# Performance work log

Hardware: AMD Instinct MI355X
Metric: run time of the kernel (lower is better)

Reference implementation:

```python
import jax, jax.numpy as jnp
import numpy as np

EPS = 1e-12
W_MAX = 0.8
ALPHA_MAX = 1.5
T = 10
ETA = 0.2
ALPHA_SCALE = 1.0
N = 50000
IN_DIM = 512
HID = 256
C = 8
EH = 64
E2 = 400000  # undirected pairs; E = 2*E2 directed edges


def setup_inputs() -> dict:
    key = jax.random.key(0)
    ks = jax.random.split(key, 12)
    x = jax.random.normal(ks[0], (N, IN_DIM), jnp.float32)
    src0 = jax.random.randint(ks[1], (E2,), 0, N)
    dst0 = jax.random.randint(ks[2], (E2,), 0, N)
    edge_index = jnp.concatenate([jnp.stack([src0, dst0]), jnp.stack([dst0, src0])], axis=1)
    rev = jnp.concatenate([jnp.arange(E2) + E2, jnp.arange(E2)])
    def lin(k, i, o):
        return jax.random.normal(k, (i, o), jnp.float32) * (2.0 / i) ** 0.5
    enc_w1 = lin(ks[3], IN_DIM, HID); enc_b1 = jnp.zeros((HID,), jnp.float32)
    enc_w2 = lin(ks[4], HID, C); enc_b2 = jnp.zeros((C,), jnp.float32)
    edge_w1 = lin(ks[5], 2 * HID + 2, EH); edge_b1 = jnp.zeros((EH,), jnp.float32)
    edge_w2 = lin(ks[6], EH, 1); edge_b2 = jnp.zeros((1,), jnp.float32)
    bound = (6.0 / (C + C)) ** 0.5  # xavier_uniform
    R_raw = jax.random.uniform(ks[7], (C, C), jnp.float32, -bound, bound) + 0.5 * jnp.eye(C, dtype=jnp.float32)
    R_scale_log = jnp.float32(0.0)
    msg_logit = jnp.float32(-3.0)
    return dict(x=x, edge_index=edge_index, rev=rev,
                enc_w1=enc_w1, enc_b1=enc_b1, enc_w2=enc_w2, enc_b2=enc_b2,
                edge_w1=edge_w1, edge_b1=edge_b1, edge_w2=edge_w2, edge_b2=edge_b2,
                R_raw=R_raw, R_scale_log=R_scale_log, msg_logit=msg_logit)


def reference(x, edge_index, rev, enc_w1, enc_b1, enc_w2, enc_b2,
              edge_w1, edge_b1, edge_w2, edge_b2, R_raw, R_scale_log, msg_logit):
    num_nodes = x.shape[0]
    src, dst = edge_index[0], edge_index[1]
    # unary encoder (mlp type, eval mode -> no dropout)
    h = jax.nn.relu(x @ enc_w1 + enc_b1)
    logits = h @ enc_w2 + enc_b2
    log_phi = jax.nn.log_softmax(logits, axis=-1)  # [N, C]
    # structural edge features from out-degree of src
    deg = jax.ops.segment_sum(jnp.ones_like(src, jnp.float32), src, num_segments=num_nodes)
    logdeg = jnp.log(deg + 1.0)
    a, b = logdeg[src], logdeg[dst]
    struct = jnp.stack([a + b, jnp.abs(a - b)], axis=-1)  # [E, 2]
    # learned symmetric edge weights -> per-edge kernel K
    hs, hd = h[src], h[dst]
    edge_in = jnp.concatenate([hs * hd, jnp.abs(hs - hd), struct], axis=-1)  # [E, 2H+2]
    eh = jax.nn.relu(edge_in @ edge_w1 + edge_b1)
    w_raw = (eh @ edge_w2 + edge_b2)[:, 0]
    w = W_MAX * jax.nn.sigmoid(w_raw)
    w = 0.5 * (w + w[rev])
    R = 0.5 * (R_raw + R_raw.T)
    R = (jax.nn.softplus(R_scale_log) + 1e-06) * jnp.tanh(R)
    K = jnp.exp(w[:, None, None] * R[None])  # [E, C, C]
    degc = jnp.maximum(deg, 1.0)
    edge_norm = (degc[src] * degc[dst]) ** -0.5  # [E]
    alpha = ALPHA_MAX * jax.nn.sigmoid(msg_logit) * ALPHA_SCALE
    lp_src = log_phi[src]
    m = jax.nn.softmax(lp_src, axis=-1)  # init_unary=True

    def step(m, _):
        f = jnp.einsum('ec,ecd->ed', m, K)
        log_f = jnp.log(jnp.maximum(f, EPS)) * edge_norm[:, None]
        sum_in = jax.ops.segment_sum(log_f, dst, num_segments=num_nodes)
        excl = sum_in[src] - log_f[rev]
        m_new = jax.nn.softmax(lp_src + alpha * excl, axis=-1)
        m = (1.0 - ETA) * m + ETA * m_new
        m = jnp.maximum(m, EPS)
        m = m / m.sum(axis=-1, keepdims=True)
        return m, None

    m, _ = jax.lax.scan(step, m, None, length=T)
    # beliefs
    f = jnp.einsum('ec,ecd->ed', m, K)
    log_f = jnp.log(jnp.maximum(f, EPS)) * edge_norm[:, None]
    sum_in = jax.ops.segment_sum(log_f, dst, num_segments=num_nodes)
    beliefs = jax.nn.softmax(log_phi + alpha * sum_in, axis=-1)
    return beliefs
```

## Files before the change

kernel.cpp:

```cpp
#include <hip/hip_runtime.h>
#include <cstddef>
#include <cstdint>

typedef _Float16 h4 __attribute__((ext_vector_type(4)));
typedef _Float16 h8 __attribute__((ext_vector_type(8)));
typedef float    f4 __attribute__((ext_vector_type(4)));
typedef int      i4 __attribute__((ext_vector_type(4)));

#define NN      50000
#define IND     512
#define HIDN    256
#define E2P     400000
#define EDD     800000
#define NBLK    196
#define SCN     50176
#define EBLK    1563

#define OFF_HF16    ((size_t)0)
#define OFF_LOGF    ((size_t)0)
#define OFF_Z       ((size_t)25600000)
#define OFF_DEG     ((size_t)28800000)
#define OFF_LOGDEG  ((size_t)29004800)
#define OFF_DEGC    ((size_t)29204800)
#define OFF_BASE    ((size_t)29404800)
#define OFF_CNT     ((size_t)29609600)
#define OFF_BLK     ((size_t)29814400)
#define OFF_WT      ((size_t)29818496)
#define OFF_BT      ((size_t)30080640)
#define OFF_RS      ((size_t)30150272)
#define OFF_WSYM    ((size_t)30150784)
#define OFF_POS     ((size_t)31750784)
#define OFF_ORDER   ((size_t)34950784)
#define OFF_BASE2   ((size_t)36550784)
#define OFF_OFS2    ((size_t)36755584)
#define OFF_PRC     ((size_t)36960384)
#define OFF_WN      ((size_t)43360384)
#define OFF_M       ((size_t)46560384)
#define OFF_EIS     ((size_t)59360384)
#define WS_NEED     ((size_t)62560384)

__device__ __forceinline__ int key2(int s, int d) {
    return ((s >> 10) << 10) | (d >> 6);
}

__device__ __forceinline__ int xcd_swz(int bid, int nwg) {
    int q = nwg >> 3, r = nwg & 7;
    int x = bid & 7, idx = bid >> 3;
    return (x < r ? x * (q + 1) : r * (q + 1) + (x - r) * q) + idx;
}

__global__ void k_deg(const int* __restrict__ ei, int* __restrict__ deg,
                      int* __restrict__ cnt2) {
    int e = blockIdx.x * 256 + threadIdx.x;
    int v = ei[e];
    atomicAdd(&deg[v], 1);
    if (e < E2P) {
        int d = ei[EDD + e];
        atomicAdd(&cnt2[key2(v, d)], 1);
    }
}

__global__ void k_node(const int* __restrict__ deg, float* __restrict__ logdeg,
                       float* __restrict__ degc) {
    int n = blockIdx.x * 256 + threadIdx.x;
    if (n < NN) {
        float d = (float)deg[n];
        logdeg[n] = logf(d + 1.0f);
        degc[n]   = fmaxf(d, 1.0f);
    }
}

__global__ void k_scan1(const int* __restrict__ deg, int* __restrict__ incl,
                        int* __restrict__ blk) {
    __shared__ int sm[256];
    int i = blockIdx.x * 256 + threadIdx.x;
    int v = deg[i];
    sm[threadIdx.x] = v;
    __syncthreads();
    for (int off = 1; off < 256; off <<= 1) {
        int t = (threadIdx.x >= off) ? sm[threadIdx.x - off] : 0;
        __syncthreads();
        sm[threadIdx.x] += t;
        __syncthreads();
    }
    incl[i] = sm[threadIdx.x];
    if (threadIdx.x == 255) blk[blockIdx.x] = sm[255];
}

__global__ void k_scan2(int* __restrict__ blk) {
    __shared__ int sm[256];
    int v = (threadIdx.x < NBLK) ? blk[threadIdx.x] : 0;
    sm[threadIdx.x] = v;
    __syncthreads();
    for (int off = 1; off < 256; off <<= 1) {
        int t = (threadIdx.x >= off) ? sm[threadIdx.x - off] : 0;
        __syncthreads();
        sm[threadIdx.x] += t;
        __syncthreads();
    }
    if (threadIdx.x < NBLK) blk[threadIdx.x] = sm[threadIdx.x];
}

__global__ void k_scan3(const int* __restrict__ incl, const int* __restrict__ deg,
                        const int* __restrict__ blk, int* __restrict__ base) {
    int i = blockIdx.x * 256 + threadIdx.x;
    int off = (blockIdx.x > 0) ? blk[blockIdx.x - 1] : 0;
    base[i] = off + incl[i] - deg[i];
}

__global__ void k_pos(const int* __restrict__ ei, const int* __restrict__ base,
                      int* __restrict__ cnt, int* __restrict__ pos) {
    int e = blockIdx.x * 256 + threadIdx.x;
    int dstn = ei[EDD + e];
    pos[e] = base[dstn] + atomicAdd(&cnt[dstn], 1);
}

__global__ void k_order(const int* __restrict__ ei, const int* __restrict__ base2,
                        int* __restrict__ ofs2, int* __restrict__ order) {
    int p = blockIdx.x * 256 + threadIdx.x;
    if (p < E2P) {
        int k = key2(ei[p], ei[EDD + p]);
        order[base2[k] + atomicAdd(&ofs2[k], 1)] = p;
    }
}

__global__ void k_gath(const int* __restrict__ ei, const int* __restrict__ order,
                       int2* __restrict__ eiS) {
    int i = blockIdx.x * 256 + threadIdx.x;
    if (i < E2P) {
        int p = order[i];
        eiS[i] = make_int2(ei[p], ei[EDD + p]);
    }
}

__global__ void k_prep(const float* __restrict__ enc_w1, const float* __restrict__ edge_w1,
                       const float* __restrict__ R_raw, const float* __restrict__ Rsl,
                       const float* __restrict__ mlog,
                       _Float16* __restrict__ Wt, _Float16* __restrict__ Bt,
                       float* __restrict__ Rs) {
    int gid = blockIdx.x * 256 + threadIdx.x;
    if (gid < 256 * 512) {
        int n = gid >> 9, k = gid & 511;
        Wt[n * 512 + k] = (_Float16)enc_w1[k * 256 + n];
        return;
    }
    int g2 = gid - 256 * 512;
    if (g2 < 64 * 544) {
        int n = g2 / 544, k = g2 - n * 544;
        float v = 0.0f;
        if (k < 512) {
            int tm = k >> 5, r = k & 31;
            int qq = r >> 3, jj = (r >> 1) & 3, typ = k & 1;
            int c = (tm >> 1) * 32 + qq * 8 + (tm & 1) * 4 + jj;
            v = edge_w1[(typ ? 256 + c : c) * 64 + n];
        } else if (k < 514) {
            v = edge_w1[k * 64 + n];
        }
        Bt[n * 544 + k] = (_Float16)v;
        return;
    }
    int g3 = g2 - 64 * 544;
    if (g3 < 64) {
        int c = g3 >> 3, d = g3 & 7;
        float rv = 0.5f * (R_raw[c * 8 + d] + R_raw[d * 8 + c]);
        float s  = log1pf(expf(Rsl[0])) + 1e-6f;
        Rs[g3] = s * tanhf(rv);
        return;
    }
    if (g3 == 64) {
        Rs[64] = 1.5f / (1.0f + expf(-mlog[0]));
    }
}

__global__ __launch_bounds__(256) void k_enc(const float* __restrict__ x,
                                             const _Float16* __restrict__ Wt,
                                             const float* __restrict__ b1,
                                             _Float16* __restrict__ hf) {
    __shared__ _Float16 XL[32 * 32];
    __shared__ _Float16 WL[256 * 32];
    const int tid = threadIdx.x;
    const int wid = tid >> 6;
    const int lane = tid & 63;
    const int l15 = lane & 15;
    const int q = lane >> 4;
    const int m0 = blockIdx.x * 32;
    const int mt = wid & 1;
    const int nh = wid >> 1;

    f4 acc[8];
#pragma unroll
    for (int i = 0; i < 8; i++) acc[i] = (f4){0.f, 0.f, 0.f, 0.f};

    const int xr = tid >> 2;
    const int xs = tid & 3;
    const bool xact = (tid < 128);
    const int gr = m0 + xr;

    h8 xreg = (h8){0, 0, 0, 0, 0, 0, 0, 0};
    if (xact && gr < NN) {
        const f4* xp = (const f4*)(x + (size_t)gr * IND + xs * 8);
        f4 a0 = xp[0], a1 = xp[1];
#pragma unroll
        for (int u = 0; u < 4; u++) { xreg[u] = (_Float16)a0[u]; xreg[4 + u] = (_Float16)a1[u]; }
    }
    h8 wreg[4];
#pragma unroll
    for (int rep = 0; rep < 4; rep++) {
        int id = rep * 256 + tid;
        int n = id >> 2, c = id & 3;
        wreg[rep] = *(const h8*)(Wt + (size_t)n * IND + c * 8);
    }

    for (int kt = 0; kt < 16; kt++) {
        __syncthreads();
        if (xact) *(h8*)&XL[xr * 32 + ((xs + (xr >> 1)) & 3) * 8] = xreg;
#pragma unroll
        for (int rep = 0; rep < 4; rep++) {
            int id = rep * 256 + tid;
            int n = id >> 2, c = id & 3;
            *(h8*)&WL[n * 32 + ((c + (n >> 1)) & 3) * 8] = wreg[rep];
        }
        __syncthreads();
        if (kt < 15) {
            const int kc = (kt + 1) * 32;
            if (xact && gr < NN) {
                const f4* xp = (const f4*)(x + (size_t)gr * IND + kc + xs * 8);
                f4 a0 = xp[0], a1 = xp[1];
#pragma unroll
                for (int u = 0; u < 4; u++) { xreg[u] = (_Float16)a0[u]; xreg[4 + u] = (_Float16)a1[u]; }
            }
#pragma unroll
            for (int rep = 0; rep < 4; rep++) {
                int id = rep * 256 + tid;
                int n = id >> 2, c = id & 3;
                wreg[rep] = *(const h8*)(Wt + (size_t)n * IND + kc + c * 8);
            }
        }
        const int ar = mt * 16 + l15;
        h8 a = *(const h8*)&XL[ar * 32 + ((q + (ar >> 1)) & 3) * 8];
#pragma unroll
        for (int nt8 = 0; nt8 < 8; nt8++) {
            int r2 = (nh * 8 + nt8) * 16 + l15;
            h8 b = *(const h8*)&WL[r2 * 32 + ((q + (r2 >> 1)) & 3) * 8];
            acc[nt8] = __builtin_amdgcn_mfma_f32_16x16x32_f16(a, b, acc[nt8], 0, 0, 0);
        }
    }
#pragma unroll
    for (int nt8 = 0; nt8 < 8; nt8++) {
        int col = (nh * 8 + nt8) * 16 + l15;
        float bv = b1[col];
#pragma unroll
        for (int reg = 0; reg < 4; reg++) {
            int row = m0 + mt * 16 + q * 4 + reg;
            if (row < NN) {
                float v = acc[nt8][reg] + bv;
                hf[(size_t)row * HIDN + col] = (_Float16)fmaxf(v, 0.f);
            }
        }
    }
}

__global__ void k_logits(const _Float16* __restrict__ hf, const float* __restrict__ w2,
                         const float* __restrict__ b2, float* __restrict__ Z) {
    __shared__ float w2L[2048];
    for (int i = threadIdx.x; i < 2048; i += 256) w2L[i] = w2[i];
    __syncthreads();
    int n = blockIdx.x * 256 + threadIdx.x;
    if (n >= NN) return;
    float sum[8];
#pragma unroll
    for (int c = 0; c < 8; c++) sum[c] = b2[c];
    for (int kb = 0; kb < 32; kb++) {
        h8 hv = *(const h8*)(hf + (size_t)n * HIDN + kb * 8);
#pragma unroll
        for (int u = 0; u < 8; u++) {
            float hx = (float)hv[u];
            const float* wr = &w2L[(kb * 8 + u) * 8];
#pragma unroll
            for (int c = 0; c < 8; c++) sum[c] += hx * wr[c];
        }
    }
    float mx = sum[0];
#pragma unroll
    for (int c = 1; c < 8; c++) mx = fmaxf(mx, sum[c]);
    float se = 0.f;
#pragma unroll
    for (int c = 0; c < 8; c++) se += __expf(sum[c] - mx);
    float lse = __logf(se);
#pragma unroll
    for (int c = 0; c < 8; c++) Z[(size_t)n * 16 + c] = sum[c] - mx - lse;
}

__global__ __launch_bounds__(256) void k_edge(const int2* __restrict__ eiS,
        const _Float16* __restrict__ hf, const float* __restrict__ logdeg,
        const _Float16* __restrict__ BtG, const float* __restrict__ eb1,
        const float* __restrict__ ew2, const float* __restrict__ eb2,
        float* __restrict__ wsym2) {
    __shared__ _Float16 BtL[64 * 136];
    const int tid = threadIdx.x;
    const int wid = tid >> 6;
    const int lane = tid & 63;
    const int l15 = lane & 15;
    const int q = lane >> 4;
    const int eb = xcd_swz(blockIdx.x, gridDim.x) * 128;

    int sidx[2], didx[2];
    float la[2], lb[2];
#pragma unroll
    for (int mt = 0; mt < 2; mt++) {
        int e = eb + wid * 32 + mt * 16 + l15;
        int2 sd = eiS[e];
        sidx[mt] = sd.x;
        didx[mt] = sd.y;
        la[mt] = logdeg[sidx[mt]];
        lb[mt] = logdeg[didx[mt]];
    }

    f4 acc[2][4];
#pragma unroll
    for (int a = 0; a < 2; a++)
#pragma unroll
        for (int b = 0; b < 4; b++) acc[a][b] = (f4){0.f, 0.f, 0.f, 0.f};

    const _Float16* hq = hf + q * 8;
    h8 curS[2], curD[2];
#pragma unroll
    for (int mt = 0; mt < 2; mt++) {
        curS[mt] = *(const h8*)(hq + (size_t)sidx[mt] * HIDN);
        curD[mt] = *(const h8*)(hq + (size_t)didx[mt] * HIDN);
    }

    for (int ph = 0; ph < 4; ph++) {
        __syncthreads();
        {
            const int r = tid >> 2;
            const int c0 = tid & 3;
            const int kbase = ph * 128;
#pragma unroll
            for (int i2 = 0; i2 < 4; i2++) {
                int ck = c0 + i2 * 4;
                *(h8*)&BtL[r * 136 + ck * 8] =
                    *(const h8*)(BtG + (size_t)r * 544 + kbase + ck * 8);
            }
        }
        __syncthreads();
#pragma unroll
        for (int kk2 = 0; kk2 < 2; kk2++) {
            const int kk = ph * 2 + kk2;
            h8 nxtS[2], nxtD[2];
            if (kk < 7) {
                const int c1 = (kk + 1) * 32;
#pragma unroll
                for (int mt = 0; mt < 2; mt++) {
                    nxtS[mt] = *(const h8*)(hq + (size_t)sidx[mt] * HIDN + c1);
                    nxtD[mt] = *(const h8*)(hq + (size_t)didx[mt] * HIDN + c1);
                }
            }
            const int ko = kk2 * 64 + q * 8;
            {
                h8 a0[2];
#pragma unroll
                for (int mt = 0; mt < 2; mt++) {
#pragma unroll
                    for (int j = 0; j < 4; j++) {
                        float x1 = (float)curS[mt][j], x2 = (float)curD[mt][j];
                        a0[mt][2 * j]     = (_Float16)(x1 * x2);
                        a0[mt][2 * j + 1] = (_Float16)fabsf(x1 - x2);
                    }
                }
                h8 bf[4];
#pragma unroll
                for (int nt = 0; nt < 4; nt++)
                    bf[nt] = *(const h8*)&BtL[(nt * 16 + l15) * 136 + ko];
#pragma unroll
                for (int mt = 0; mt < 2; mt++)
#pragma unroll
                    for (int nt = 0; nt < 4; nt++)
                        acc[mt][nt] = __builtin_amdgcn_mfma_f32_16x16x32_f16(a0[mt], bf[nt], acc[mt][nt], 0, 0, 0);
            }
            {
                h8 a1[2];
#pragma unroll
                for (int mt = 0; mt < 2; mt++) {
#pragma unroll
                    for (int j = 0; j < 4; j++) {
                        float x1 = (float)curS[mt][4 + j], x2 = (float)curD[mt][4 + j];
                        a1[mt][2 * j]     = (_Float16)(x1 * x2);
                        a1[mt][2 * j + 1] = (_Float16)fabsf(x1 - x2);
                    }
                }
                h8 bf[4];
#pragma unroll
                for (int nt = 0; nt < 4; nt++)
                    bf[nt] = *(const h8*)&BtL[(nt * 16 + l15) * 136 + ko + 32];
#pragma unroll
                for (int mt = 0; mt < 2; mt++)
#pragma unroll
                    for (int nt = 0; nt < 4; nt++)
                        acc[mt][nt] = __builtin_amdgcn_mfma_f32_16x16x32_f16(a1[mt], bf[nt], acc[mt][nt], 0, 0, 0);
            }
            if (kk < 7) {
#pragma unroll
                for (int mt = 0; mt < 2; mt++) { curS[mt] = nxtS[mt]; curD[mt] = nxtD[mt]; }
            }
        }
    }

    __syncthreads();
    {
        const int r = tid >> 2, ck = tid & 3;
        *(h8*)&BtL[r * 136 + ck * 8] = *(const h8*)(BtG + (size_t)r * 544 + 512 + ck * 8);
    }
    __syncthreads();
    {
        h8 bf[4];
#pragma unroll
        for (int nt = 0; nt < 4; nt++)
            bf[nt] = *(const h8*)&BtL[(nt * 16 + l15) * 136 + q * 8];
#pragma unroll
        for (int mt = 0; mt < 2; mt++) {
            h8 a = (h8){0, 0, 0, 0, 0, 0, 0, 0};
            if (q == 0) {
                a[0] = (_Float16)(la[mt] + lb[mt]);
                a[1] = (_Float16)fabsf(la[mt] - lb[mt]);
            }
#pragma unroll
            for (int nt = 0; nt < 4; nt++)
                acc[mt][nt] = __builtin_amdgcn_mfma_f32_16x16x32_f16(a, bf[nt], acc[mt][nt], 0, 0, 0);
        }
    }

    float b1v[4], w2v[4];
#pragma unroll
    for (int nt = 0; nt < 4; nt++) {
        int col = nt * 16 + l15;
        b1v[nt] = eb1[col];
        w2v[nt] = ew2[col];
    }
    const float b2s = eb2[0];
    float part[2][4];
#pragma unroll
    for (int mt = 0; mt < 2; mt++)
#pragma unroll
        for (int reg = 0; reg < 4; reg++) {
            float s = 0.f;
#pragma unroll
            for (int nt = 0; nt < 4; nt++) {
                float v = acc[mt][nt][reg] + b1v[nt];
                s += fmaxf(v, 0.f) * w2v[nt];
            }
            part[mt][reg] = s;
        }
#pragma unroll
    for (int off = 1; off < 16; off <<= 1)
#pragma unroll
        for (int mt = 0; mt < 2; mt++)
#pragma unroll
            for (int reg = 0; reg < 4; reg++)
                part[mt][reg] += __shfl_xor(part[mt][reg], off, 64);
    if (l15 == 0) {
#pragma unroll
        for (int mt = 0; mt < 2; mt++)
#pragma unroll
            for (int reg = 0; reg < 4; reg++) {
                int er = eb + wid * 32 + mt * 16 + q * 4 + reg;
                if (er < E2P) {
                    float xr = part[mt][reg] + b2s;
                    wsym2[er] = 0.8f / (1.0f + __expf(-xr));
                }
            }
    }
}


__device__ __forceinline__ void kprod(const float* __restrict__ RsL, float w,
                                      const float* me, const float* mr,
                                      float* fe, float* fr) {
#pragma unroll
    for (int d = 0; d < 8; d++) { fe[d] = 0.f; fr[d] = 0.f; }
#pragma unroll
    for (int c = 0; c < 8; c++) {
        {
            float kv = __expf(w * RsL[c * 8 + c]);
            fe[c] += me[c] * kv;
            fr[c] += mr[c] * kv;
        }
#pragma unroll
        for (int d = c + 1; d < 8; d++) {
            float kv = __expf(w * RsL[c * 8 + d]);
            fe[d] += me[c] * kv; fr[d] += mr[c] * kv;
            fe[c] += me[d] * kv; fr[c] += mr[d] * kv;
        }
    }
}

__global__ __launch_bounds__(256) void k_init(const int2* __restrict__ eiS,
        const float* __restrict__ wsym2, const float* __restrict__ degc,
        const float* __restrict__ Rs, const float* __restrict__ Z,
        const int* __restrict__ pos, const int* __restrict__ order,
        i4* __restrict__ prc, float2* __restrict__ wn,
        _Float16* __restrict__ M, _Float16* __restrict__ logf) {
    __shared__ float RsL[64];
    const int tid = threadIdx.x;
    if (tid < 64) RsL[tid] = Rs[tid];
    __syncthreads();
    int i = xcd_swz(blockIdx.x, EBLK) * 256 + tid;
    if (i >= E2P) return;
    int p = order[i];
    int2 sd = eiS[i];
    int sp = sd.x, dp = sd.y;
    float w = wsym2[i];
    float nrm = rsqrtf(degc[sp] * degc[dp]);
    int pz0 = pos[p], pz1 = pos[E2P + p];
    prc[i] = (i4){sp, dp, pz0, pz1};
    wn[i] = make_float2(w, nrm);
    const f4* Zs = (const f4*)(Z + (size_t)sp * 16);
    const f4* Zd = (const f4*)(Z + (size_t)dp * 16);
    f4 ls0 = Zs[0], ls1 = Zs[1], ld0 = Zd[0], ld1 = Zd[1];
    float lps[8], lpd[8];
#pragma unroll
    for (int u = 0; u < 4; u++) { lps[u] = ls0[u]; lps[4+u] = ls1[u]; lpd[u] = ld0[u]; lpd[4+u] = ld1[u]; }
    float me[8], mr[8];
    {
        float mx = lps[0], mx2 = lpd[0];
#pragma unroll
        for (int d = 1; d < 8; d++) { mx = fmaxf(mx, lps[d]); mx2 = fmaxf(mx2, lpd[d]); }
        float s = 0.f, s2 = 0.f;
#pragma unroll
        for (int d = 0; d < 8; d++) { me[d] = __expf(lps[d] - mx); s += me[d];
                                      mr[d] = __expf(lpd[d] - mx2); s2 += mr[d]; }
        float rs = 1.f / s, rs2 = 1.f / s2;
#pragma unroll
        for (int d = 0; d < 8; d++) { me[d] *= rs; mr[d] *= rs2; }
    }
    {
        h8 mh, mh2;
#pragma unroll
        for (int d = 0; d < 8; d++) { mh[d] = (_Float16)me[d]; mh2[d] = (_Float16)mr[d]; }
        *(h8*)(M + (size_t)i * 16)     = mh;
        *(h8*)(M + (size_t)i * 16 + 8) = mh2;
    }
    float fe[8], fr[8];
    kprod(RsL, w, me, mr, fe, fr);
    h8 le, lr;
#pragma unroll
    for (int d = 0; d < 8; d++) {
        le[d] = (_Float16)(__logf(fmaxf(fe[d], 1e-12f)) * nrm);
        lr[d] = (_Float16)(__logf(fmaxf(fr[d], 1e-12f)) * nrm);
    }
    *(h8*)(logf + (size_t)pz0 * 8) = le;
    *(h8*)(logf + (size_t)pz1 * 8) = lr;
}

__global__ __launch_bounds__(256) void k_bpF(const i4* __restrict__ prc,
        const float2* __restrict__ wn, const float* __restrict__ Rs,
        const float* __restrict__ Z, _Float16* __restrict__ M,
        _Float16* __restrict__ logf) {
    __shared__ float RsL[64];
    const int tid = threadIdx.x;
    if (tid < 64) RsL[tid] = Rs[tid];
    __syncthreads();
    int i = xcd_swz(blockIdx.x, EBLK) * 256 + tid;
    if (i >= E2P) return;
    i4 c4 = prc[i];
    const int sp = c4[0], dp = c4[1], pz0 = c4[2], pz1 = c4[3];
    float2 wnv = wn[i];
    const float w = wnv.x, nrm = wnv.y;
    const float alpha = Rs[64];
    h8 mhe = *(const h8*)(M + (size_t)i * 16);
    h8 mhr = *(const h8*)(M + (size_t)i * 16 + 8);
    float me[8], mr[8];
#pragma unroll
    for (int d = 0; d < 8; d++) { me[d] = (float)mhe[d]; mr[d] = (float)mhr[d]; }
    float fe[8], fr[8];
    kprod(RsL, w, me, mr, fe, fr);
    float lfe[8], lfr[8];
#pragma unroll
    for (int d = 0; d < 8; d++) {
        lfe[d] = __logf(fmaxf(fe[d], 1e-12f)) * nrm;
        lfr[d] = __logf(fmaxf(fr[d], 1e-12f)) * nrm;
    }
    const f4* Zs = (const f4*)(Z + (size_t)sp * 16);
    const f4* Zd = (const f4*)(Z + (size_t)dp * 16);
    f4 ls0 = Zs[0], ls1 = Zs[1], ss0 = Zs[2], ss1 = Zs[3];
    f4 ld0 = Zd[0], ld1 = Zd[1], sd0 = Zd[2], sd1 = Zd[3];
    float te[8], tr[8];
#pragma unroll
    for (int u = 0; u < 4; u++) {
        te[u]     = ls0[u] + alpha * (ss0[u] - lfr[u]);
        te[4 + u] = ls1[u] + alpha * (ss1[u] - lfr[4 + u]);
        tr[u]     = ld0[u] + alpha * (sd0[u] - lfe[u]);
        tr[4 + u] = ld1[u] + alpha * (sd1[u] - lfe[4 + u]);
    }
    float m1[8], m2[8];
    {
        float mx = te[0], mx2 = tr[0];
#pragma unroll
        for (int d = 1; d < 8; d++) { mx = fmaxf(mx, te[d]); mx2 = fmaxf(mx2, tr[d]); }
        float s = 0.f, s2 = 0.f;
#pragma unroll
        for (int d = 0; d < 8; d++) { m1[d] = __expf(te[d] - mx); s += m1[d];
                                      m2[d] = __expf(tr[d] - mx2); s2 += m2[d]; }
        float rs = 1.f / s, rs2 = 1.f / s2;
        float t1 = 0.f, t2 = 0.f;
#pragma unroll
        for (int d = 0; d < 8; d++) {
            m1[d] = fmaxf(0.8f * me[d] + 0.2f * m1[d] * rs, 1e-12f);  t1 += m1[d];
            m2[d] = fmaxf(0.8f * mr[d] + 0.2f * m2[d] * rs2, 1e-12f); t2 += m2[d];
        }
        float rt1 = 1.f / t1, rt2 = 1.f / t2;
#pragma unroll
        for (int d = 0; d < 8; d++) { m1[d] *= rt1; m2[d] *= rt2; }
    }
    {
        h8 mh, mh2;
#pragma unroll
        for (int d = 0; d < 8; d++) { mh[d] = (_Float16)m1[d]; mh2[d] = (_Float16)m2[d]; }
        *(h8*)(M + (size_t)i * 16)     = mh;
        *(h8*)(M + (size_t)i * 16 + 8) = mh2;
    }
    float fe2[8], fr2[8];
    kprod(RsL, w, m1, m2, fe2, fr2);
    h8 le, lr;
#pragma unroll
    for (int d = 0; d < 8; d++) {
        le[d] = (_Float16)(__logf(fmaxf(fe2[d], 1e-12f)) * nrm);
        lr[d] = (_Float16)(__logf(fmaxf(fr2[d], 1e-12f)) * nrm);
    }
    *(h8*)(logf + (size_t)pz0 * 8) = le;
    *(h8*)(logf + (size_t)pz1 * 8) = lr;
}

__global__ void k_sum(const _Float16* __restrict__ logf, const int* __restrict__ base,
                      const int* __restrict__ deg, float* __restrict__ Z,
                      const float* __restrict__ Rs, float* __restrict__ out, int fin) {
    int g = blockIdx.x * 256 + threadIdx.x;
    int n = g >> 3;
    if (n >= NN) return;
    int j = threadIdx.x & 7;
    int b = base[n], cnt = deg[n];
    float acc[8];
#pragma unroll
    for (int d = 0; d < 8; d++) acc[d] = 0.f;
    for (int s = j; s < cnt; s += 8) {
        h8 v = *(const h8*)(logf + (size_t)(b + s) * 8);
#pragma unroll
        for (int d = 0; d < 8; d++) acc[d] += (float)v[d];
    }
    int lane = threadIdx.x & 63;
    float v4[4], v2[2], r;
    {
        bool hi = (lane & 4) != 0;
#pragma unroll
        for (int i = 0; i < 4; i++) {
            float send = hi ? acc[i] : acc[i + 4];
            float recv = __shfl_xor(send, 4, 64);
            v4[i] = (hi ? acc[i + 4] : acc[i]) + recv;
        }
    }
    {
        bool hi = (lane & 2) != 0;
#pragma unroll
        for (int i = 0; i < 2; i++) {
            float send = hi ? v4[i] : v4[i + 2];
            float recv = __shfl_xor(send, 2, 64);
            v2[i] = (hi ? v4[i + 2] : v4[i]) + recv;
        }
    }
    {
        bool hi = (lane & 1) != 0;
        float send = hi ? v2[0] : v2[1];
        float recv = __shfl_xor(send, 1, 64);
        r = (hi ? v2[1] : v2[0]) + recv;
    }
    if (!fin) {
        Z[(size_t)n * 16 + 8 + j] = r;
    } else {
        float alpha = Rs[64];
        float v = Z[(size_t)n * 16 + j] + alpha * r;
        float mx = v;
        mx = fmaxf(mx, __shfl_xor(mx, 1, 64));
        mx = fmaxf(mx, __shfl_xor(mx, 2, 64));
        mx = fmaxf(mx, __shfl_xor(mx, 4, 64));
        float ex = __expf(v - mx);
        float s = ex;
        s += __shfl_xor(s, 1, 64); s += __shfl_xor(s, 2, 64); s += __shfl_xor(s, 4, 64);
        out[(size_t)n * 8 + j] = ex / s;
    }
}

extern "C" void kernel_launch(void* const* d_in, const int* in_sizes, int n_in,
                              void* d_out, int out_size, void* d_ws, size_t ws_size,
                              hipStream_t stream) {
    if (ws_size < WS_NEED) return;
    const float* x        = (const float*)d_in[0];
    const int*   ei       = (const int*)d_in[1];
    const float* enc_w1   = (const float*)d_in[3];
    const float* enc_b1   = (const float*)d_in[4];
    const float* enc_w2   = (const float*)d_in[5];
    const float* enc_b2   = (const float*)d_in[6];
    const float* edge_w1  = (const float*)d_in[7];
    const float* edge_b1  = (const float*)d_in[8];
    const float* edge_w2  = (const float*)d_in[9];
    const float* edge_b2  = (const float*)d_in[10];
    const float* R_raw    = (const float*)d_in[11];
    const float* Rsl      = (const float*)d_in[12];
    const float* mlog     = (const float*)d_in[13];

    char* ws = (char*)d_ws;
    _Float16* hf     = (_Float16*)(ws + OFF_HF16);
    _Float16* logfb  = (_Float16*)(ws + OFF_LOGF);
    float* Zb        = (float*)(ws + OFF_Z);
    int*   deg       = (int*)  (ws + OFF_DEG);
    float* logdeg    = (float*)(ws + OFF_LOGDEG);
    float* degc      = (float*)(ws + OFF_DEGC);
    int*   baseA     = (int*)  (ws + OFF_BASE);
    int*   cnt       = (int*)  (ws + OFF_CNT);
    int*   blk       = (int*)  (ws + OFF_BLK);
    _Float16* Wt     = (_Float16*)(ws + OFF_WT);
    _Float16* Bt     = (_Float16*)(ws + OFF_BT);
    float* Rs        = (float*)(ws + OFF_RS);
    float* wsym2     = (float*)(ws + OFF_WSYM);
    int*   pos       = (int*)  (ws + OFF_POS);
    int*   order     = (int*)  (ws + OFF_ORDER);
    int*   base2     = (int*)  (ws + OFF_BASE2);
    int*   ofs2      = (int*)  (ws + OFF_OFS2);
    i4*    prc       = (i4*)   (ws + OFF_PRC);
    float2* wnb      = (float2*)(ws + OFF_WN);
    _Float16* Mb     = (_Float16*)(ws + OFF_M);
    int2*  eiS       = (int2*) (ws + OFF_EIS);
    float* outp      = (float*)d_out;

    hipMemsetAsync(deg, 0, (size_t)SCN * 4, stream);
    hipMemsetAsync(ofs2, 0, (size_t)SCN * 4, stream);
    k_deg<<<dim3(EDD / 256), dim3(256), 0, stream>>>(ei, deg, ofs2);
    k_node<<<dim3(NBLK), dim3(256), 0, stream>>>(deg, logdeg, degc);
    k_prep<<<dim3((256 * 512 + 64 * 544 + 65 + 255) / 256), dim3(256), 0, stream>>>(
        enc_w1, edge_w1, R_raw, Rsl, mlog, Wt, Bt, Rs);
    k_scan1<<<dim3(NBLK), dim3(256), 0, stream>>>(deg, cnt , blk);
    k_scan2<<<dim3(1), dim3(256), 0, stream>>>(blk);
    k_scan3<<<dim3(NBLK), dim3(256), 0, stream>>>(cnt, deg, blk, baseA);
    hipMemsetAsync(cnt, 0, (size_t)SCN * 4, stream);
    k_pos<<<dim3(EDD / 256), dim3(256), 0, stream>>>(ei, baseA, cnt, pos);
    k_scan1<<<dim3(NBLK), dim3(256), 0, stream>>>(ofs2, cnt, blk);
    k_scan2<<<dim3(1), dim3(256), 0, stream>>>(blk);
    k_scan3<<<dim3(NBLK), dim3(256), 0, stream>>>(cnt, ofs2, blk, base2);
    hipMemsetAsync(ofs2, 0, (size_t)SCN * 4, stream);
    k_order<<<dim3(EBLK), dim3(256), 0, stream>>>(ei, base2, ofs2, order);
    k_gath<<<dim3(EBLK), dim3(256), 0, stream>>>(ei, order, eiS);
    k_enc<<<dim3((NN + 31) / 32), dim3(256), 0, stream>>>(x, Wt, enc_b1, hf);
    k_logits<<<dim3(NBLK), dim3(256), 0, stream>>>(hf, enc_w2, enc_b2, Zb);
    k_edge<<<dim3(E2P / 128), dim3(256), 0, stream>>>(eiS, hf, logdeg, Bt, edge_b1,
                                                      edge_w2, edge_b2, wsym2);
    k_init<<<dim3(EBLK), dim3(256), 0, stream>>>(eiS, wsym2, degc, Rs, Zb, pos, order,
                                                 prc, wnb, Mb, logfb);
    k_sum<<<dim3((NN * 8 + 255) / 256), dim3(256), 0, stream>>>(logfb, baseA, deg, Zb,
                                                                Rs, outp, 0);
    for (int t = 0; t < 10; t++) {
        k_bpF<<<dim3(EBLK), dim3(256), 0, stream>>>(prc, wnb, Rs, Zb, Mb, logfb);
        k_sum<<<dim3((NN * 8 + 255) / 256), dim3(256), 0, stream>>>(logfb, baseA, deg, Zb,
                                                                    Rs, outp, (t == 9) ? 1 : 0);
    }
    (void)in_sizes; (void)n_in; (void)out_size;
}
```

Before: 806.4 us.

## Split BP message update to one thread per directed edge and retile encoder GEMM

The belief-propagation step kernel now runs one thread per directed edge instead of one per undirected pair. Each thread reads a packed 16-byte record holding node, position, weight and norm, and gets the reverse edge's log-factor from its neighbour lane through a shuffle. This doubles the thread count and cuts per-thread register pressure, at the cost of recomputing the reverse message's log and doubling record storage. Separately, the encoder GEMM moves to 64-row blocks where each wave keeps its X fragment in registers, with a double-buffered padded LDS tile for the weights. That removes the X LDS staging and one barrier per k-step.

```diff
diff --git a/kernel.cpp b/kernel.cpp
--- a/kernel.cpp
+++ b/kernel.cpp
@@ -15,6 +15,7 @@
 #define NBLK    196
 #define SCN     50176
 #define EBLK    1563
+#define DBLK    3125
 
 #define OFF_HF16    ((size_t)0)
 #define OFF_LOGF    ((size_t)0)
@@ -33,11 +34,10 @@
 #define OFF_ORDER   ((size_t)34950784)
 #define OFF_BASE2   ((size_t)36550784)
 #define OFF_OFS2    ((size_t)36755584)
-#define OFF_PRC     ((size_t)36960384)
-#define OFF_WN      ((size_t)43360384)
-#define OFF_M       ((size_t)46560384)
-#define OFF_EIS     ((size_t)59360384)
-#define WS_NEED     ((size_t)62560384)
+#define OFF_EIS     ((size_t)36960384)
+#define OFF_M2      ((size_t)40160384)
+#define OFF_REC     ((size_t)52960384)
+#define WS_NEED     ((size_t)65760384)
 
 __device__ __forceinline__ int key2(int s, int d) {
     return ((s >> 10) << 10) | (d >> 6);
@@ -176,85 +176,72 @@
                                              const _Float16* __restrict__ Wt,
                                              const float* __restrict__ b1,
                                              _Float16* __restrict__ hf) {
-    __shared__ _Float16 XL[32 * 32];
-    __shared__ _Float16 WL[256 * 32];
+    __shared__ _Float16 WL[2][256 * 40];
     const int tid = threadIdx.x;
     const int wid = tid >> 6;
     const int lane = tid & 63;
     const int l15 = lane & 15;
     const int q = lane >> 4;
-    const int m0 = blockIdx.x * 32;
-    const int mt = wid & 1;
-    const int nh = wid >> 1;
-
-    f4 acc[8];
-#pragma unroll
-    for (int i = 0; i < 8; i++) acc[i] = (f4){0.f, 0.f, 0.f, 0.f};
-
-    const int xr = tid >> 2;
-    const int xs = tid & 3;
-    const bool xact = (tid < 128);
-    const int gr = m0 + xr;
-
-    h8 xreg = (h8){0, 0, 0, 0, 0, 0, 0, 0};
-    if (xact && gr < NN) {
-        const f4* xp = (const f4*)(x + (size_t)gr * IND + xs * 8);
-        f4 a0 = xp[0], a1 = xp[1];
-#pragma unroll
-        for (int u = 0; u < 4; u++) { xreg[u] = (_Float16)a0[u]; xreg[4 + u] = (_Float16)a1[u]; }
-    }
+    const int m0 = blockIdx.x * 64;
+    const int row = m0 + wid * 16 + l15;
+    const bool ract = (row < NN);
+    const float* xrow = x + (size_t)row * IND;
+
+    f4 acc[16];
+#pragma unroll
+    for (int i = 0; i < 16; i++) acc[i] = (f4){0.f, 0.f, 0.f, 0.f};
+
+    const int wn  = tid >> 2;
+    const int wo  = (tid & 3) * 8;
+
     h8 wreg[4];
 #pragma unroll
-    for (int rep = 0; rep < 4; rep++) {
-        int id = rep * 256 + tid;
-        int n = id >> 2, c = id & 3;
-        wreg[rep] = *(const h8*)(Wt + (size_t)n * IND + c * 8);
+    for (int rep = 0; rep < 4; rep++)
+        wreg[rep] = *(const h8*)(Wt + (size_t)(rep * 64 + wn) * IND + wo);
+    f4 xa = (f4){0, 0, 0, 0}, xb = (f4){0, 0, 0, 0};
+    if (ract) {
+        const f4* xp = (const f4*)(xrow + q * 8);
+        xa = xp[0]; xb = xp[1];
     }
 
     for (int kt = 0; kt < 16; kt++) {
+        const int cur = kt & 1;
+#pragma unroll
+        for (int rep = 0; rep < 4; rep++)
+            *(h8*)&WL[cur][(rep * 64 + wn) * 40 + wo] = wreg[rep];
         __syncthreads();
-        if (xact) *(h8*)&XL[xr * 32 + ((xs + (xr >> 1)) & 3) * 8] = xreg;
-#pragma unroll
-        for (int rep = 0; rep < 4; rep++) {
-            int id = rep * 256 + tid;
-            int n = id >> 2, c = id & 3;
-            *(h8*)&WL[n * 32 + ((c + (n >> 1)) & 3) * 8] = wreg[rep];
-        }
-        __syncthreads();
+        f4 xa2, xb2;
         if (kt < 15) {
             const int kc = (kt + 1) * 32;
-            if (xact && gr < NN) {
-                const f4* xp = (const f4*)(x + (size_t)gr * IND + kc + xs * 8);
-                f4 a0 = xp[0], a1 = xp[1];
-#pragma unroll
-                for (int u = 0; u < 4; u++) { xreg[u] = (_Float16)a0[u]; xreg[4 + u] = (_Float16)a1[u]; }
-            }
-#pragma unroll
-            for (int rep = 0; rep < 4; rep++) {
-                int id = rep * 256 + tid;
-                int n = id >> 2, c = id & 3;
-                wreg[rep] = *(const h8*)(Wt + (size_t)n * IND + kc + c * 8);
-            }
-        }
-        const int ar = mt * 16 + l15;
-        h8 a = *(const h8*)&XL[ar * 32 + ((q + (ar >> 1)) & 3) * 8];
-#pragma unroll
-        for (int nt8 = 0; nt8 < 8; nt8++) {
-            int r2 = (nh * 8 + nt8) * 16 + l15;
-            h8 b = *(const h8*)&WL[r2 * 32 + ((q + (r2 >> 1)) & 3) * 8];
-            acc[nt8] = __builtin_amdgcn_mfma_f32_16x16x32_f16(a, b, acc[nt8], 0, 0, 0);
-        }
-    }
-#pragma unroll
-    for (int nt8 = 0; nt8 < 8; nt8++) {
-        int col = (nh * 8 + nt8) * 16 + l15;
+#pragma unroll
+            for (int rep = 0; rep < 4; rep++)
+                wreg[rep] = *(const h8*)(Wt + (size_t)(rep * 64 + wn) * IND + kc + wo);
+            if (ract) {
+                const f4* xp = (const f4*)(xrow + kc + q * 8);
+                xa2 = xp[0]; xb2 = xp[1];
+            }
+        }
+        h8 a;
+#pragma unroll
+        for (int u = 0; u < 4; u++) { a[u] = (_Float16)xa[u]; a[4 + u] = (_Float16)xb[u]; }
+#pragma unroll
+        for (int nt = 0; nt < 16; nt++) {
+            h8 b = *(const h8*)&WL[cur][(nt * 16 + l15) * 40 + q * 8];
+            acc[nt] = __builtin_amdgcn_mfma_f32_16x16x32_f16(a, b, acc[nt], 0, 0, 0);
+        }
+        if (kt < 15 && ract) { xa = xa2; xb = xb2; }
+        __syncthreads();
+    }
+#pragma unroll
+    for (int nt = 0; nt < 16; nt++) {
+        int col = nt * 16 + l15;
         float bv = b1[col];
 #pragma unroll
         for (int reg = 0; reg < 4; reg++) {
-            int row = m0 + mt * 16 + q * 4 + reg;
-            if (row < NN) {
-                float v = acc[nt8][reg] + bv;
-                hf[(size_t)row * HIDN + col] = (_Float16)fmaxf(v, 0.f);
+            int orow = m0 + wid * 16 + q * 4 + reg;
+            if (orow < NN) {
+                float v = acc[nt][reg] + bv;
+                hf[(size_t)orow * HIDN + col] = (_Float16)fmaxf(v, 0.f);
             }
         }
     }
@@ -473,23 +460,21 @@
 }
 
 
-__device__ __forceinline__ void kprod(const float* __restrict__ RsL, float w,
-                                      const float* me, const float* mr,
-                                      float* fe, float* fr) {
-#pragma unroll
-    for (int d = 0; d < 8; d++) { fe[d] = 0.f; fr[d] = 0.f; }
+__device__ __forceinline__ void kprod1(const float* __restrict__ RsL, float w,
+                                       const float* m, float* f) {
+#pragma unroll
+    for (int d = 0; d < 8; d++) f[d] = 0.f;
 #pragma unroll
     for (int c = 0; c < 8; c++) {
         {
             float kv = __expf(w * RsL[c * 8 + c]);
-            fe[c] += me[c] * kv;
-            fr[c] += mr[c] * kv;
+            f[c] += m[c] * kv;
         }
 #pragma unroll
         for (int d = c + 1; d < 8; d++) {
             float kv = __expf(w * RsL[c * 8 + d]);
-            fe[d] += me[c] * kv; fr[d] += mr[c] * kv;
-            fe[c] += me[d] * kv; fr[c] += mr[d] * kv;
+            f[d] += m[c] * kv;
+            f[c] += m[d] * kv;
         }
     }
 }
@@ -498,8 +483,8 @@
         const float* __restrict__ wsym2, const float* __restrict__ degc,
         const float* __restrict__ Rs, const float* __restrict__ Z,
         const int* __restrict__ pos, const int* __restrict__ order,
-        i4* __restrict__ prc, float2* __restrict__ wn,
-        _Float16* __restrict__ M, _Float16* __restrict__ logf) {
+        i4* __restrict__ rec, _Float16* __restrict__ M2,
+        _Float16* __restrict__ logf) {
     __shared__ float RsL[64];
     const int tid = threadIdx.x;
     if (tid < 64) RsL[tid] = Rs[tid];
@@ -512,8 +497,8 @@
     float w = wsym2[i];
     float nrm = rsqrtf(degc[sp] * degc[dp]);
     int pz0 = pos[p], pz1 = pos[E2P + p];
-    prc[i] = (i4){sp, dp, pz0, pz1};
-    wn[i] = make_float2(w, nrm);
+    rec[2 * i]     = (i4){sp, pz0, (int)__float_as_int(w), (int)__float_as_int(nrm)};
+    rec[2 * i + 1] = (i4){dp, pz1, (int)__float_as_int(w), (int)__float_as_int(nrm)};
     const f4* Zs = (const f4*)(Z + (size_t)sp * 16);
     const f4* Zd = (const f4*)(Z + (size_t)dp * 16);
     f4 ls0 = Zs[0], ls1 = Zs[1], ld0 = Zd[0], ld1 = Zd[1];
@@ -537,11 +522,12 @@
         h8 mh, mh2;
 #pragma unroll
         for (int d = 0; d < 8; d++) { mh[d] = (_Float16)me[d]; mh2[d] = (_Float16)mr[d]; }
-        *(h8*)(M + (size_t)i * 16)     = mh;
-        *(h8*)(M + (size_t)i * 16 + 8) = mh2;
+        *(h8*)(M2 + (size_t)(2 * i) * 8)     = mh;
+        *(h8*)(M2 + (size_t)(2 * i + 1) * 8) = mh2;
     }
     float fe[8], fr[8];
-    kprod(RsL, w, me, mr, fe, fr);
+    kprod1(RsL, w, me, fe);
+    kprod1(RsL, w, mr, fr);
     h8 le, lr;
 #pragma unroll
     for (int d = 0; d < 8; d++) {
@@ -552,83 +538,68 @@
     *(h8*)(logf + (size_t)pz1 * 8) = lr;
 }
 
-__global__ __launch_bounds__(256) void k_bpF(const i4* __restrict__ prc,
-        const float2* __restrict__ wn, const float* __restrict__ Rs,
-        const float* __restrict__ Z, _Float16* __restrict__ M,
-        _Float16* __restrict__ logf) {
+__global__ __launch_bounds__(256) void k_bp2(const i4* __restrict__ rec,
+        const float* __restrict__ Rs, const float* __restrict__ Z,
+        _Float16* __restrict__ M2, _Float16* __restrict__ logf) {
     __shared__ float RsL[64];
     const int tid = threadIdx.x;
     if (tid < 64) RsL[tid] = Rs[tid];
     __syncthreads();
-    int i = xcd_swz(blockIdx.x, EBLK) * 256 + tid;
-    if (i >= E2P) return;
-    i4 c4 = prc[i];
-    const int sp = c4[0], dp = c4[1], pz0 = c4[2], pz1 = c4[3];
-    float2 wnv = wn[i];
-    const float w = wnv.x, nrm = wnv.y;
+    const int qq = xcd_swz(blockIdx.x, DBLK) * 256 + tid;
+    i4 r = rec[qq];
+    const int node = r[0], pz = r[1];
+    const float w = __int_as_float(r[2]), nrm = __int_as_float(r[3]);
     const float alpha = Rs[64];
-    h8 mhe = *(const h8*)(M + (size_t)i * 16);
-    h8 mhr = *(const h8*)(M + (size_t)i * 16 + 8);
-    float me[8], mr[8];
-#pragma unroll
-    for (int d = 0; d < 8; d++) { me[d] = (float)mhe[d]; mr[d] = (float)mhr[d]; }
-    float fe[8], fr[8];
-    kprod(RsL, w, me, mr, fe, fr);
-    float lfe[8], lfr[8];
-#pragma unroll
-    for (int d = 0; d < 8; d++) {
-        lfe[d] = __logf(fmaxf(fe[d], 1e-12f)) * nrm;
-        lfr[d] = __logf(fmaxf(fr[d], 1e-12f)) * nrm;
-    }
-    const f4* Zs = (const f4*)(Z + (size_t)sp * 16);
-    const f4* Zd = (const f4*)(Z + (size_t)dp * 16);
-    f4 ls0 = Zs[0], ls1 = Zs[1], ss0 = Zs[2], ss1 = Zs[3];
-    f4 ld0 = Zd[0], ld1 = Zd[1], sd0 = Zd[2], sd1 = Zd[3];
-    float te[8], tr[8];
+    h8 mh = *(const h8*)(M2 + (size_t)qq * 8);
+    float m[8];
+#pragma unroll
+    for (int d = 0; d < 8; d++) m[d] = (float)mh[d];
+    float f[8];
+    kprod1(RsL, w, m, f);
+    float lf[8], lfo[8];
+#pragma unroll
+    for (int d = 0; d < 8; d++) lf[d] = __logf(fmaxf(f[d], 1e-12f)) * nrm;
+#pragma unroll
+    for (int d = 0; d < 8; d++) lfo[d] = __shfl_xor(lf[d], 1, 64);
+    const f4* Zr = (const f4*)(Z + (size_t)node * 16);
+    f4 z0 = Zr[0], z1 = Zr[1], z2 = Zr[2], z3 = Zr[3];
+    float t[8];
 #pragma unroll
     for (int u = 0; u < 4; u++) {
-        te[u]     = ls0[u] + alpha * (ss0[u] - lfr[u]);
-        te[4 + u] = ls1[u] + alpha * (ss1[u] - lfr[4 + u]);
-        tr[u]     = ld0[u] + alpha * (sd0[u] - lfe[u]);
-        tr[4 + u] = ld1[u] + alpha * (sd1[u] - lfe[4 + u]);
-    }
-    float m1[8], m2[8];
-    {
-        float mx = te[0], mx2 = tr[0];
-#pragma unroll
-        for (int d = 1; d < 8; d++) { mx = fmaxf(mx, te[d]); mx2 = fmaxf(mx2, tr[d]); }
-        float s = 0.f, s2 = 0.f;
-#pragma unroll
-        for (int d = 0; d < 8; d++) { m1[d] = __expf(te[d] - mx); s += m1[d];
-                                      m2[d] = __expf(tr[d] - mx2); s2 += m2[d]; }
-        float rs = 1.f / s, rs2 = 1.f / s2;
-        float t1 = 0.f, t2 = 0.f;
+        t[u]     = z0[u] + alpha * (z2[u] - lfo[u]);
+        t[4 + u] = z1[u] + alpha * (z3[u] - lfo[4 + u]);
+    }
+    float m1[8];
+    {
+        float mx = t[0];
+#pragma unroll
+        for (int d = 1; d < 8; d++) mx = fmaxf(mx, t[d]);
+        float s = 0.f;
+#pragma unroll
+        for (int d = 0; d < 8; d++) { m1[d] = __expf(t[d] - mx); s += m1[d]; }
+        float rs = 1.f / s;
+        float t1 = 0.f;
 #pragma unroll
         for (int d = 0; d < 8; d++) {
-            m1[d] = fmaxf(0.8f * me[d] + 0.2f * m1[d] * rs, 1e-12f);  t1 += m1[d];
-            m2[d] = fmaxf(0.8f * mr[d] + 0.2f * m2[d] * rs2, 1e-12f); t2 += m2[d];
-        }
-        float rt1 = 1.f / t1, rt2 = 1.f / t2;
-#pragma unroll
-        for (int d = 0; d < 8; d++) { m1[d] *= rt1; m2[d] *= rt2; }
-    }
-    {
-        h8 mh, mh2;
-#pragma unroll
-        for (int d = 0; d < 8; d++) { mh[d] = (_Float16)m1[d]; mh2[d] = (_Float16)m2[d]; }
-        *(h8*)(M + (size_t)i * 16)     = mh;
-        *(h8*)(M + (size_t)i * 16 + 8) = mh2;
-    }
-    float fe2[8], fr2[8];
-    kprod(RsL, w, m1, m2, fe2, fr2);
-    h8 le, lr;
-#pragma unroll
-    for (int d = 0; d < 8; d++) {
-        le[d] = (_Float16)(__logf(fmaxf(fe2[d], 1e-12f)) * nrm);
-        lr[d] = (_Float16)(__logf(fmaxf(fr2[d], 1e-12f)) * nrm);
-    }
-    *(h8*)(logf + (size_t)pz0 * 8) = le;
-    *(h8*)(logf + (size_t)pz1 * 8) = lr;
+            m1[d] = fmaxf(0.8f * m[d] + 0.2f * m1[d] * rs, 1e-12f); t1 += m1[d];
+        }
+        float rt = 1.f / t1;
+#pragma unroll
+        for (int d = 0; d < 8; d++) m1[d] *= rt;
+    }
+    {
+        h8 mo;
+#pragma unroll
+        for (int d = 0; d < 8; d++) mo[d] = (_Float16)m1[d];
+        *(h8*)(M2 + (size_t)qq * 8) = mo;
+    }
+    float f2[8];
+    kprod1(RsL, w, m1, f2);
+    h8 le;
+#pragma unroll
+    for (int d = 0; d < 8; d++)
+        le[d] = (_Float16)(__logf(fmaxf(f2[d], 1e-12f)) * nrm);
+    *(h8*)(logf + (size_t)pz * 8) = le;
 }
 
 __global__ void k_sum(const _Float16* __restrict__ logf, const int* __restrict__ base,
@@ -725,10 +696,9 @@
     int*   order     = (int*)  (ws + OFF_ORDER);
     int*   base2     = (int*)  (ws + OFF_BASE2);
     int*   ofs2      = (int*)  (ws + OFF_OFS2);
-    i4*    prc       = (i4*)   (ws + OFF_PRC);
-    float2* wnb      = (float2*)(ws + OFF_WN);
-    _Float16* Mb     = (_Float16*)(ws + OFF_M);
     int2*  eiS       = (int2*) (ws + OFF_EIS);
+    _Float16* M2b    = (_Float16*)(ws + OFF_M2);
+    i4*    rec       = (i4*)   (ws + OFF_REC);
     float* outp      = (float*)d_out;
 
     hipMemsetAsync(deg, 0, (size_t)SCN * 4, stream);
@@ -748,16 +718,16 @@
     hipMemsetAsync(ofs2, 0, (size_t)SCN * 4, stream);
     k_order<<<dim3(EBLK), dim3(256), 0, stream>>>(ei, base2, ofs2, order);
     k_gath<<<dim3(EBLK), dim3(256), 0, stream>>>(ei, order, eiS);
-    k_enc<<<dim3((NN + 31) / 32), dim3(256), 0, stream>>>(x, Wt, enc_b1, hf);
+    k_enc<<<dim3((NN + 63) / 64), dim3(256), 0, stream>>>(x, Wt, enc_b1, hf);
     k_logits<<<dim3(NBLK), dim3(256), 0, stream>>>(hf, enc_w2, enc_b2, Zb);
     k_edge<<<dim3(E2P / 128), dim3(256), 0, stream>>>(eiS, hf, logdeg, Bt, edge_b1,
                                                       edge_w2, edge_b2, wsym2);
     k_init<<<dim3(EBLK), dim3(256), 0, stream>>>(eiS, wsym2, degc, Rs, Zb, pos, order,
-                                                 prc, wnb, Mb, logfb);
+                                                 rec, M2b, logfb);
     k_sum<<<dim3((NN * 8 + 255) / 256), dim3(256), 0, stream>>>(logfb, baseA, deg, Zb,
                                                                 Rs, outp, 0);
     for (int t = 0; t < 10; t++) {
-        k_bpF<<<dim3(EBLK), dim3(256), 0, stream>>>(prc, wnb, Rs, Zb, Mb, logfb);
+        k_bp2<<<dim3(DBLK), dim3(256), 0, stream>>>(rec, Rs, Zb, M2b, logfb);
         k_sum<<<dim3((NN * 8 + 255) / 256), dim3(256), 0, stream>>>(logfb, baseA, deg, Zb,
                                                                     Rs, outp, (t == 9) ? 1 : 0);
     }
```

Result: no change. 816.6 us (+1.3%).

## Fuse logits/log-softmax into encoder GEMM with 64-row tiles and double-buffered weights

Applied to the files above, without the earlier changes.

The encoder kernel now handles 64 rows per block with each wave computing a full 16x256 output strip. X is loaded straight from global memory into MFMA A-operand registers, which removes the X shared-memory tile. The weight tile is double-buffered in padded LDS, so each k-step needs one barrier instead of two. The second-layer logits and log-softmax are computed from the accumulators with a cross-lane shuffle reduction, which removes the separate k_logits kernel and its re-read of h. In exchange, the kernel holds more accumulator registers and launches half as many blocks.

```diff
diff --git a/kernel.cpp b/kernel.cpp
--- a/kernel.cpp
+++ b/kernel.cpp
@@ -173,122 +173,139 @@
 }
 
 __global__ __launch_bounds__(256) void k_enc(const float* __restrict__ x,
-                                             const _Float16* __restrict__ Wt,
-                                             const float* __restrict__ b1,
-                                             _Float16* __restrict__ hf) {
-    __shared__ _Float16 XL[32 * 32];
-    __shared__ _Float16 WL[256 * 32];
+        const _Float16* __restrict__ Wt, const float* __restrict__ b1,
+        const float* __restrict__ w2, const float* __restrict__ b2,
+        _Float16* __restrict__ hf, float* __restrict__ Z) {
+    __shared__ _Float16 WL[2][256 * 40];
     const int tid = threadIdx.x;
     const int wid = tid >> 6;
     const int lane = tid & 63;
     const int l15 = lane & 15;
     const int q = lane >> 4;
-    const int m0 = blockIdx.x * 32;
-    const int mt = wid & 1;
-    const int nh = wid >> 1;
-
-    f4 acc[8];
-#pragma unroll
-    for (int i = 0; i < 8; i++) acc[i] = (f4){0.f, 0.f, 0.f, 0.f};
-
-    const int xr = tid >> 2;
-    const int xs = tid & 3;
-    const bool xact = (tid < 128);
-    const int gr = m0 + xr;
-
-    h8 xreg = (h8){0, 0, 0, 0, 0, 0, 0, 0};
-    if (xact && gr < NN) {
-        const f4* xp = (const f4*)(x + (size_t)gr * IND + xs * 8);
-        f4 a0 = xp[0], a1 = xp[1];
-#pragma unroll
-        for (int u = 0; u < 4; u++) { xreg[u] = (_Float16)a0[u]; xreg[4 + u] = (_Float16)a1[u]; }
-    }
+    const int m0 = blockIdx.x * 64;
+    const int row = m0 + wid * 16 + l15;
+    const bool ract = (row < NN);
+    const float* xrow = x + (size_t)row * IND;
+
+    f4 acc[16];
+#pragma unroll
+    for (int i = 0; i < 16; i++) acc[i] = (f4){0.f, 0.f, 0.f, 0.f};
+
+    const int wn = tid >> 2;
+    const int wo = (tid & 3) * 8;
+
     h8 wreg[4];
 #pragma unroll
-    for (int rep = 0; rep < 4; rep++) {
-        int id = rep * 256 + tid;
-        int n = id >> 2, c = id & 3;
-        wreg[rep] = *(const h8*)(Wt + (size_t)n * IND + c * 8);
+    for (int rep = 0; rep < 4; rep++)
+        wreg[rep] = *(const h8*)(Wt + (size_t)(rep * 64 + wn) * IND + wo);
+    f4 xa = (f4){0, 0, 0, 0}, xb = (f4){0, 0, 0, 0};
+    if (ract) {
+        const f4* xp = (const f4*)(xrow + q * 8);
+        xa = xp[0]; xb = xp[1];
     }
 
     for (int kt = 0; kt < 16; kt++) {
+        const int cur = kt & 1;
+#pragma unroll
+        for (int rep = 0; rep < 4; rep++)
+            *(h8*)&WL[cur][(rep * 64 + wn) * 40 + wo] = wreg[rep];
         __syncthreads();
-        if (xact) *(h8*)&XL[xr * 32 + ((xs + (xr >> 1)) & 3) * 8] = xreg;
-#pragma unroll
-        for (int rep = 0; rep < 4; rep++) {
-            int id = rep * 256 + tid;
-            int n = id >> 2, c = id & 3;
-            *(h8*)&WL[n * 32 + ((c + (n >> 1)) & 3) * 8] = wreg[rep];
-        }
-        __syncthreads();
+        f4 xa2, xb2;
         if (kt < 15) {
             const int kc = (kt + 1) * 32;
-            if (xact && gr < NN) {
-                const f4* xp = (const f4*)(x + (size_t)gr * IND + kc + xs * 8);
-                f4 a0 = xp[0], a1 = xp[1];
-#pragma unroll
-                for (int u = 0; u < 4; u++) { xreg[u] = (_Float16)a0[u]; xreg[4 + u] = (_Float16)a1[u]; }
-            }
-#pragma unroll
-            for (int rep = 0; rep < 4; rep++) {
-                int id = rep * 256 + tid;
-                int n = id >> 2, c = id & 3;
-                wreg[rep] = *(const h8*)(Wt + (size_t)n * IND + kc + c * 8);
-            }
-        }
-        const int ar = mt * 16 + l15;
-        h8 a = *(const h8*)&XL[ar * 32 + ((q + (ar >> 1)) & 3) * 8];
-#pragma unroll
-        for (int nt8 = 0; nt8 < 8; nt8++) {
-            int r2 = (nh * 8 + nt8) * 16 + l15;
-            h8 b = *(const h8*)&WL[r2 * 32 + ((q + (r2 >> 1)) & 3) * 8];
-            acc[nt8] = __builtin_amdgcn_mfma_f32_16x16x32_f16(a, b, acc[nt8], 0, 0, 0);
-        }
-    }
-#pragma unroll
-    for (int nt8 = 0; nt8 < 8; nt8++) {
-        int col = (nh * 8 + nt8) * 16 + l15;
-        float bv = b1[col];
+#pragma unroll
+            for (int rep = 0; rep < 4; rep++)
+                wreg[rep] = *(const h8*)(Wt + (size_t)(rep * 64 + wn) * IND + kc + wo);
+            if (ract) {
+                const f4* xp = (const f4*)(xrow + kc + q * 8);
+                xa2 = xp[0]; xb2 = xp[1];
+            }
+        }
+        h8 a;
+#pragma unroll
+        for (int u = 0; u < 4; u++) { a[u] = (_Float16)xa[u]; a[4 + u] = (_Float16)xb[u]; }
+#pragma unroll
+        for (int nt = 0; nt < 16; nt++) {
+            h8 b = *(const h8*)&WL[cur][(nt * 16 + l15) * 40 + q * 8];
+            acc[nt] = __builtin_amdgcn_mfma_f32_16x16x32_f16(a, b, acc[nt], 0, 0, 0);
+        }
+        if (kt < 15 && ract) { xa = xa2; xb = xb2; }
+        __syncthreads();
+    }
+
+    float bv16[16];
+#pragma unroll
+    for (int nt = 0; nt < 16; nt++) bv16[nt] = b1[nt * 16 + l15];
+#pragma unroll
+    for (int nt = 0; nt < 16; nt++) {
+        int col = nt * 16 + l15;
 #pragma unroll
         for (int reg = 0; reg < 4; reg++) {
-            int row = m0 + mt * 16 + q * 4 + reg;
-            if (row < NN) {
-                float v = acc[nt8][reg] + bv;
-                hf[(size_t)row * HIDN + col] = (_Float16)fmaxf(v, 0.f);
-            }
-        }
-    }
-}
-
-__global__ void k_logits(const _Float16* __restrict__ hf, const float* __restrict__ w2,
-                         const float* __restrict__ b2, float* __restrict__ Z) {
-    __shared__ float w2L[2048];
-    for (int i = threadIdx.x; i < 2048; i += 256) w2L[i] = w2[i];
+            int orow = m0 + wid * 16 + q * 4 + reg;
+            if (orow < NN) {
+                float v = acc[nt][reg] + bv16[nt];
+                hf[(size_t)orow * HIDN + col] = (_Float16)fmaxf(v, 0.f);
+            }
+        }
+    }
+    float* w2L = (float*)&WL[0][0];
     __syncthreads();
-    int n = blockIdx.x * 256 + threadIdx.x;
-    if (n >= NN) return;
-    float sum[8];
-#pragma unroll
-    for (int c = 0; c < 8; c++) sum[c] = b2[c];
-    for (int kb = 0; kb < 32; kb++) {
-        h8 hv = *(const h8*)(hf + (size_t)n * HIDN + kb * 8);
-#pragma unroll
-        for (int u = 0; u < 8; u++) {
-            float hx = (float)hv[u];
-            const float* wr = &w2L[(kb * 8 + u) * 8];
-#pragma unroll
-            for (int c = 0; c < 8; c++) sum[c] += hx * wr[c];
-        }
-    }
-    float mx = sum[0];
-#pragma unroll
-    for (int c = 1; c < 8; c++) mx = fmaxf(mx, sum[c]);
-    float se = 0.f;
-#pragma unroll
-    for (int c = 0; c < 8; c++) se += __expf(sum[c] - mx);
-    float lse = __logf(se);
-#pragma unroll
-    for (int c = 0; c < 8; c++) Z[(size_t)n * 16 + c] = sum[c] - mx - lse;
+    for (int i2 = tid; i2 < 2048; i2 += 256) w2L[i2] = w2[i2];
+    __syncthreads();
+    float lsum[4][8];
+#pragma unroll
+    for (int r2 = 0; r2 < 4; r2++)
+#pragma unroll
+        for (int c = 0; c < 8; c++) lsum[r2][c] = 0.f;
+#pragma unroll
+    for (int nt = 0; nt < 16; nt++) {
+        const float* wr = &w2L[(nt * 16 + l15) * 8];
+        f4 w0 = *(const f4*)wr;
+        f4 w1 = *(const f4*)(wr + 4);
+#pragma unroll
+        for (int r2 = 0; r2 < 4; r2++) {
+            float v = fmaxf(acc[nt][r2] + bv16[nt], 0.f);
+            float hx = (float)(_Float16)v;
+#pragma unroll
+            for (int c = 0; c < 4; c++) {
+                lsum[r2][c]     += hx * w0[c];
+                lsum[r2][4 + c] += hx * w1[c];
+            }
+        }
+    }
+#pragma unroll
+    for (int off = 1; off < 16; off <<= 1)
+#pragma unroll
+        for (int r2 = 0; r2 < 4; r2++)
+#pragma unroll
+            for (int c = 0; c < 8; c++)
+                lsum[r2][c] += __shfl_xor(lsum[r2][c], off, 64);
+    if (l15 == 0) {
+#pragma unroll
+        for (int r2 = 0; r2 < 4; r2++) {
+            int orow = m0 + wid * 16 + q * 4 + r2;
+            if (orow < NN) {
+                float s8[8];
+#pragma unroll
+                for (int c = 0; c < 8; c++) s8[c] = lsum[r2][c] + b2[c];
+                float mx = s8[0];
+#pragma unroll
+                for (int c = 1; c < 8; c++) mx = fmaxf(mx, s8[c]);
+                float se = 0.f;
+#pragma unroll
+                for (int c = 0; c < 8; c++) se += __expf(s8[c] - mx);
+                float lse = __logf(se);
+                f4 z0, z1;
+#pragma unroll
+                for (int c = 0; c < 4; c++) {
+                    z0[c] = s8[c] - mx - lse;
+                    z1[c] = s8[4 + c] - mx - lse;
+                }
+                *(f4*)(Z + (size_t)orow * 16)     = z0;
+                *(f4*)(Z + (size_t)orow * 16 + 4) = z1;
+            }
+        }
+    }
 }
 
 __global__ __launch_bounds__(256) void k_edge(const int2* __restrict__ eiS,
@@ -748,8 +765,8 @@
     hipMemsetAsync(ofs2, 0, (size_t)SCN * 4, stream);
     k_order<<<dim3(EBLK), dim3(256), 0, stream>>>(ei, base2, ofs2, order);
     k_gath<<<dim3(EBLK), dim3(256), 0, stream>>>(ei, order, eiS);
-    k_enc<<<dim3((NN + 31) / 32), dim3(256), 0, stream>>>(x, Wt, enc_b1, hf);
-    k_logits<<<dim3(NBLK), dim3(256), 0, stream>>>(hf, enc_w2, enc_b2, Zb);
+    k_enc<<<dim3((NN + 63) / 64), dim3(256), 0, stream>>>(x, Wt, enc_b1, enc_w2, enc_b2,
+                                                          hf, Zb);
     k_edge<<<dim3(E2P / 128), dim3(256), 0, stream>>>(eiS, hf, logdeg, Bt, edge_b1,
                                                       edge_w2, edge_b2, wsym2);
     k_init<<<dim3(EBLK), dim3(256), 0, stream>>>(eiS, wsym2, degc, Rs, Zb, pos, order,
```

After: 805.4 us. Within noise of the previous version (-0.1%).
